# Performance work log

Measured on AMD Instinct MI355X. Metric: run time of the kernel, lower is better.

Reference implementation:

```python
import jax, jax.numpy as jnp
import numpy as np

DIM = 1024
HEADS = 16
HEAD_DIM = 64
INNER = HEADS * HEAD_DIM  # 1024
B, N = 4, 2048
EPS = 1e-5


def setup_inputs() -> dict:
    key = jax.random.key(0)
    ks = jax.random.split(key, 5)
    x = jax.random.normal(ks[0], (B, N, DIM), dtype=jnp.float32)
    w_qkv = jax.random.normal(ks[1], (DIM, 3 * INNER), dtype=jnp.float32) * (DIM ** -0.5)
    w_out = jax.random.normal(ks[2], (INNER, DIM), dtype=jnp.float32) * (INNER ** -0.5)
    b_out = jax.random.normal(ks[3], (DIM,), dtype=jnp.float32) * 0.01
    ln_gamma = jnp.ones((DIM,), dtype=jnp.float32)
    ln_beta = jnp.zeros((DIM,), dtype=jnp.float32)
    return {"x": x, "w_qkv": w_qkv, "w_out": w_out, "b_out": b_out,
            "ln_gamma": ln_gamma, "ln_beta": ln_beta}


def reference(x, w_qkv, w_out, b_out, ln_gamma, ln_beta):
    scale = HEAD_DIM ** -0.5
    qkv = x @ w_qkv  # [b, n, 3*inner]
    q, k, v = jnp.split(qkv, 3, axis=-1)
    q = q * scale
    # [b, n, h*d] -> [b, h, n, d]
    def to_heads(t):
        b, n, _ = t.shape
        return t.reshape(b, n, HEADS, HEAD_DIM).transpose(0, 2, 1, 3)
    q, k, v = to_heads(q), to_heads(k), to_heads(v)
    scores = jnp.einsum('bhid,bhjd->bhij', q, k)
    attn = jax.nn.softmax(scores, axis=-1)  # max-subtraction (detached) is internal
    out = jnp.einsum('bhij,bhjd->bhid', attn, v)
    out = out.transpose(0, 2, 1, 3).reshape(x.shape[0], x.shape[1], INNER)
    out = out @ w_out + b_out
    # LayerNorm over last dim
    mu = out.mean(axis=-1, keepdims=True)
    var = out.var(axis=-1, keepdims=True)
    out = (out - mu) * jax.lax.rsqrt(var + EPS)
    return out * ln_gamma + ln_beta
```

## Files before the change

### kernel.cpp

```cpp
#include <hip/hip_runtime.h>


typedef __bf16 bf16;
typedef __bf16 bf16x4 __attribute__((ext_vector_type(4)));
typedef __bf16 bf16x8 __attribute__((ext_vector_type(8)));
typedef float f32x4 __attribute__((ext_vector_type(4)));
typedef float f32x16 __attribute__((ext_vector_type(16)));
typedef unsigned int u32x2 __attribute__((ext_vector_type(2)));
typedef unsigned int u32x4 __attribute__((ext_vector_type(4)));

#define QSCALE_LOG2E 0.18033688011112042f

#define GLOAD_LDS16(gp, lp)                                                   \
  __builtin_amdgcn_global_load_lds(                                           \
      (const __attribute__((address_space(1))) unsigned int*)(const void*)(gp), \
      (__attribute__((address_space(3))) unsigned int*)(void*)(lp), 16, 0, 0)

__device__ __forceinline__ float fexp2(float x) {
#if __has_builtin(__builtin_amdgcn_exp2f)
  return __builtin_amdgcn_exp2f(x);
#else
  return __expf(x * 0.6931471805599453f);
#endif
}

__device__ __forceinline__ unsigned pack2t(float lo, float hi) {
  return __builtin_amdgcn_perm(__float_as_uint(hi), __float_as_uint(lo), 0x07060302u);
}

__global__ __launch_bounds__(256) void cvt_k(const float* __restrict__ in,
                                             bf16* __restrict__ out) {
  const size_t i = ((size_t)blockIdx.x * 256 + threadIdx.x) * 8;
  float4 a = *(const float4*)(in + i);
  float4 b = *(const float4*)(in + i + 4);
  bf16x8 o = {(bf16)a.x, (bf16)a.y, (bf16)a.z, (bf16)a.w,
              (bf16)b.x, (bf16)b.y, (bf16)b.z, (bf16)b.w};
  *(bf16x8*)(out + i) = o;
}

__global__ __launch_bounds__(256) void transpose_k(const float* __restrict__ in,
                                                   bf16* __restrict__ out,
                                                   int Kd, int Nd) {
  __shared__ bf16 t[32][36];
  const int n0 = blockIdx.x * 32, k0 = blockIdx.y * 32;
  const int r = threadIdx.x >> 3, c4 = (threadIdx.x & 7) * 4;
  float4 v = *(const float4*)(in + (size_t)(k0 + r) * Nd + n0 + c4);
  t[c4 + 0][r] = (bf16)v.x; t[c4 + 1][r] = (bf16)v.y;
  t[c4 + 2][r] = (bf16)v.z; t[c4 + 3][r] = (bf16)v.w;
  __syncthreads();
  bf16x4 o = *(const bf16x4*)&t[r][c4];
  *(bf16x4*)(out + (size_t)(n0 + r) * Kd + k0 + c4) = o;
}

template <bool QKV>
__global__ __launch_bounds__(256) void gemm2(const bf16* __restrict__ A,
                                             const bf16* __restrict__ Bt,
                                             bf16* __restrict__ C,
                                             bf16* __restrict__ Vt) {
  __shared__ bf16 As[128][64];
  __shared__ bf16 Bs[128][64];
  const int tid = threadIdx.x;
  const int l = tid & 63, w = tid >> 6;
  const int g = l >> 4, q = l & 15, q7 = q & 7;
  const int wm = w >> 1, wn = w & 1;
  const int m0 = blockIdx.x * 128, n0 = blockIdx.y * 128;
  const int lr = tid >> 3;
  const int sc = ((tid & 7) ^ (lr & 7)) * 8;

  f32x4 acc[4][4] = {};

  for (int k0 = 0; k0 < 1024; k0 += 64) {
    __syncthreads();
#pragma unroll
    for (int k = 0; k < 4; k++) {
      GLOAD_LDS16(A + (size_t)(m0 + lr + k * 32) * 1024 + k0 + sc,
                  &As[0][0] + tid * 8 + k * 2048);
      GLOAD_LDS16(Bt + (size_t)(n0 + lr + k * 32) * 1024 + k0 + sc,
                  &Bs[0][0] + tid * 8 + k * 2048);
    }
    __syncthreads();

#pragma unroll
    for (int ks = 0; ks < 2; ks++) {
      bf16x8 af[4], bfr[4];
#pragma unroll
      for (int mi = 0; mi < 4; mi++) {
        const int R = wm * 64 + mi * 16 + q;
        af[mi] = *(const bf16x8*)((const char*)&As[0][0] + R * 128 +
                                  (((ks * 4 + g) ^ q7) << 4));
      }
#pragma unroll
      for (int ni = 0; ni < 4; ni++) {
        const int R = wn * 64 + ni * 16 + q;
        bfr[ni] = *(const bf16x8*)((const char*)&Bs[0][0] + R * 128 +
                                   (((ks * 4 + g) ^ q7) << 4));
      }
#pragma unroll
      for (int mi = 0; mi < 4; mi++)
#pragma unroll
        for (int ni = 0; ni < 4; ni++)
          acc[mi][ni] = __builtin_amdgcn_mfma_f32_16x16x32_bf16(af[mi], bfr[ni],
                                                                acc[mi][ni], 0, 0, 0);
    }
  }

  if (QKV && n0 >= 2048) {
#pragma unroll
    for (int mi = 0; mi < 4; mi++)
#pragma unroll
      for (int ni = 0; ni < 4; ni++) {
        const int vcol = n0 - 2048 + wn * 64 + ni * 16 + q;
        const int h = vcol >> 6, d = vcol & 63;
        const int t0 = m0 + wm * 64 + mi * 16 + g * 4;
        const int b = t0 >> 11, n = t0 & 2047;
        bf16x4 o = {(bf16)acc[mi][ni][0], (bf16)acc[mi][ni][1],
                    (bf16)acc[mi][ni][2], (bf16)acc[mi][ni][3]};
        *(bf16x4*)(Vt + ((size_t)(b * 16 + h) * 64 + d) * 2048 + n) = o;
      }
  } else {
    const int ldc = QKV ? 2048 : 1024;
    const float s = (QKV && n0 < 1024) ? QSCALE_LOG2E : 1.0f;
#pragma unroll
    for (int mi = 0; mi < 4; mi++)
#pragma unroll
      for (int ni = 0; ni < 4; ni++) {
        const int col = n0 + wn * 64 + ni * 16 + q;
#pragma unroll
        for (int r = 0; r < 4; r++) {
          const int row = m0 + wm * 64 + mi * 16 + g * 4 + r;
          C[(size_t)row * ldc + col] = (bf16)(acc[mi][ni][r] * s);
        }
      }
  }
}

__global__ __launch_bounds__(256, 3) void attn_k(const bf16* __restrict__ qk,
                                                 const bf16* __restrict__ vt,
                                                 bf16* __restrict__ aout) {
  __shared__ bf16 Ks[3][64][64];
  __shared__ bf16 Vs[3][64][64];
  const int tid = threadIdx.x;
  const int l = tid & 63, w = tid >> 6;
  const int q = l & 31, hi = l >> 5, q7 = q & 7;

  const int flat = blockIdx.x;
  const int logical = (flat & 7) * 128 + (flat >> 3);
  const int qt = logical & 15, bh = logical >> 4;
  const int h = bh & 15, b = bh >> 4;
  const int qbase = qt * 128 + w * 32;

  const bf16* Kg = qk + (size_t)(b * 2048) * 2048 + 1024 + h * 64;
  const bf16* Vg = vt + ((size_t)(b * 16 + h) * 64) * 2048;

  bf16x8 qf[4];
  {
    const bf16* Qr = qk + (size_t)(b * 2048 + qbase + q) * 2048 + h * 64 + hi * 8;
#pragma unroll
    for (int i = 0; i < 4; i++) qf[i] = *(const bf16x8*)(Qr + i * 16);
  }

  const int r0 = tid >> 3, sp0 = ((tid & 7) ^ (r0 & 7)) * 8;
  const int ub = (tid >> 6) << 9;
#define STAGE_KV(buf, kt)                                                       \
  do {                                                                          \
    bf16* kd = &Ks[buf][0][0];                                                  \
    bf16* vd = &Vs[buf][0][0];                                                  \
    GLOAD_LDS16(Kg + (size_t)((kt) + r0) * 2048 + sp0, kd + ub);                \
    GLOAD_LDS16(Vg + (size_t)r0 * 2048 + (kt) + sp0, vd + ub);                  \
    GLOAD_LDS16(Kg + (size_t)((kt) + 32 + r0) * 2048 + sp0, kd + 2048 + ub);    \
    GLOAD_LDS16(Vg + (size_t)(32 + r0) * 2048 + (kt) + sp0, vd + 2048 + ub);    \
  } while (0)

#define QKT(buf, sA, sB)                                                        \
  do {                                                                          \
    const char* Kb_ = (const char*)&Ks[buf][0][0];                              \
    __builtin_amdgcn_s_setprio(1);                                              \
    {                                                                           \
      f32x16 a_ = {};                                                           \
      _Pragma("unroll")                                                         \
      for (int i = 0; i < 4; i++) {                                             \
        bf16x8 kf = *(const bf16x8*)(Kb_ + q * 128 + (((2 * i + hi) ^ q7) << 4));\
        a_ = __builtin_amdgcn_mfma_f32_32x32x16_bf16(kf, qf[i], a_, 0, 0, 0);   \
      }                                                                         \
      sA = a_;                                                                  \
    }                                                                           \
    {                                                                           \
      f32x16 a_ = {};                                                           \
      _Pragma("unroll")                                                         \
      for (int i = 0; i < 4; i++) {                                             \
        bf16x8 kf = *(const bf16x8*)(Kb_ + (32 + q) * 128 +                     \
                                     (((2 * i + hi) ^ q7) << 4));               \
        a_ = __builtin_amdgcn_mfma_f32_32x32x16_bf16(kf, qf[i], a_, 0, 0, 0);   \
      }                                                                         \
      sB = a_;                                                                  \
    }                                                                           \
    __builtin_amdgcn_s_setprio(0);                                              \
  } while (0)

  f32x16 oacc[2] = {};
  float lsA = 0.f, lsB = 0.f;

  STAGE_KV(0, 0);
  STAGE_KV(1, 64);
  asm volatile("s_waitcnt vmcnt(4)" ::: "memory");
  __builtin_amdgcn_sched_barrier(0);
  __builtin_amdgcn_s_barrier();

  f32x16 s0, s1;
  QKT(0, s0, s1);

  int cur = 0;
  for (int kt = 0; kt < 2048; kt += 64) {
    const int nbuf = (cur == 2) ? 0 : cur + 1;
    const int sbuf = (nbuf == 2) ? 0 : nbuf + 1;

    asm volatile("s_waitcnt vmcnt(0)" ::: "memory");
    __builtin_amdgcn_sched_barrier(0);
    __builtin_amdgcn_s_barrier();

    if (kt + 128 < 2048) STAGE_KV(sbuf, kt + 128);

    f32x16 n0v, n1v;
    QKT(nbuf, n0v, n1v);

#pragma unroll
    for (int r = 0; r < 16; r++) { s0[r] = fexp2(s0[r]); lsA += s0[r]; }
#pragma unroll
    for (int r = 0; r < 16; r++) { s1[r] = fexp2(s1[r]); lsB += s1[r]; }

    bf16x8 pfrag[4];
#pragma unroll
    for (int ks = 0; ks < 2; ks++) {
      const unsigned a0 = pack2t(s0[8 * ks + 0], s0[8 * ks + 1]);
      const unsigned a1 = pack2t(s0[8 * ks + 2], s0[8 * ks + 3]);
      const unsigned b0 = pack2t(s0[8 * ks + 4], s0[8 * ks + 5]);
      const unsigned b1 = pack2t(s0[8 * ks + 6], s0[8 * ks + 7]);
      u32x2 w0 = __builtin_amdgcn_permlane32_swap(a0, b0, false, false);
      u32x2 w1 = __builtin_amdgcn_permlane32_swap(a1, b1, false, false);
      u32x4 bw = {w0[0], w1[0], w0[1], w1[1]};
      pfrag[ks] = __builtin_bit_cast(bf16x8, bw);
    }
#pragma unroll
    for (int ks = 0; ks < 2; ks++) {
      const unsigned a0 = pack2t(s1[8 * ks + 0], s1[8 * ks + 1]);
      const unsigned a1 = pack2t(s1[8 * ks + 2], s1[8 * ks + 3]);
      const unsigned b0 = pack2t(s1[8 * ks + 4], s1[8 * ks + 5]);
      const unsigned b1 = pack2t(s1[8 * ks + 6], s1[8 * ks + 7]);
      u32x2 w0 = __builtin_amdgcn_permlane32_swap(a0, b0, false, false);
      u32x2 w1 = __builtin_amdgcn_permlane32_swap(a1, b1, false, false);
      u32x4 bw = {w0[0], w1[0], w0[1], w1[1]};
      pfrag[2 + ks] = __builtin_bit_cast(bf16x8, bw);
    }

    const char* Vb = (const char*)&Vs[cur][0][0];
    __builtin_amdgcn_s_setprio(1);
#pragma unroll
    for (int dblk = 0; dblk < 2; dblk++) {
      bf16x8 vfr[4];
#pragma unroll
      for (int t = 0; t < 4; t++)
        vfr[t] = *(const bf16x8*)(Vb + (dblk * 32 + q) * 128 + (((2 * t + hi) ^ q7) << 4));
#pragma unroll
      for (int t = 0; t < 4; t++)
        oacc[dblk] = __builtin_amdgcn_mfma_f32_32x32x16_bf16(vfr[t], pfrag[t],
                                                             oacc[dblk], 0, 0, 0);
    }
    __builtin_amdgcn_s_setprio(0);

    s0 = n0v; s1 = n1v;
    cur = nbuf;
  }

  float lsum = lsA + lsB;
  {
    u32x2 t2 = __builtin_amdgcn_permlane32_swap(__float_as_uint(lsum),
                                                __float_as_uint(lsum), false, false);
    lsum = __uint_as_float(t2[0]) + __uint_as_float(t2[1]);
  }
  const float inv = 1.f / lsum;
  bf16* orow = aout + (size_t)(b * 2048 + qbase + q) * 1024 + h * 64 + hi * 4;
#pragma unroll
  for (int dblk = 0; dblk < 2; dblk++)
#pragma unroll
    for (int rg = 0; rg < 4; rg++) {
      bf16x4 o = {(bf16)(oacc[dblk][4 * rg + 0] * inv), (bf16)(oacc[dblk][4 * rg + 1] * inv),
                  (bf16)(oacc[dblk][4 * rg + 2] * inv), (bf16)(oacc[dblk][4 * rg + 3] * inv)};
      *(bf16x4*)(orow + dblk * 32 + rg * 8) = o;
    }
#undef QKT
#undef STAGE_KV
}

__global__ __launch_bounds__(256) void ln_k(const bf16* __restrict__ proj,
                                            const float* __restrict__ bo,
                                            const float* __restrict__ gam,
                                            const float* __restrict__ bet,
                                            float* __restrict__ out) {
  const int tid = threadIdx.x;
  const int l = tid & 63, w = tid >> 6;
  const int row = blockIdx.x * 4 + w;
  const int c0 = l * 16;

  bf16x8 p0 = *(const bf16x8*)(proj + (size_t)row * 1024 + c0);
  bf16x8 p1 = *(const bf16x8*)(proj + (size_t)row * 1024 + c0 + 8);
  float v[16];
#pragma unroll
  for (int j = 0; j < 8; j++) { v[j] = (float)p0[j]; v[8 + j] = (float)p1[j]; }
#pragma unroll
  for (int j = 0; j < 4; j++) {
    float4 bv = *(const float4*)(bo + c0 + j * 4);
    v[4 * j + 0] += bv.x; v[4 * j + 1] += bv.y;
    v[4 * j + 2] += bv.z; v[4 * j + 3] += bv.w;
  }
  float s = 0.f, ss = 0.f;
#pragma unroll
  for (int j = 0; j < 16; j++) { s += v[j]; ss += v[j] * v[j]; }
#pragma unroll
  for (int off = 32; off > 0; off >>= 1) {
    s += __shfl_xor(s, off);
    ss += __shfl_xor(ss, off);
  }
  const float mean = s * (1.f / 1024.f);
  const float var = ss * (1.f / 1024.f) - mean * mean;
  const float rs = rsqrtf(var + 1e-5f);
#pragma unroll
  for (int j = 0; j < 4; j++) {
    float4 gv = *(const float4*)(gam + c0 + j * 4);
    float4 btv = *(const float4*)(bet + c0 + j * 4);
    float4 o;
    o.x = (v[4 * j + 0] - mean) * rs * gv.x + btv.x;
    o.y = (v[4 * j + 1] - mean) * rs * gv.y + btv.y;
    o.z = (v[4 * j + 2] - mean) * rs * gv.z + btv.z;
    o.w = (v[4 * j + 3] - mean) * rs * gv.w + btv.w;
    *(float4*)(out + (size_t)row * 1024 + c0 + j * 4) = o;
  }
}

extern "C" void kernel_launch(void* const* d_in, const int* in_sizes, int n_in,
                              void* d_out, int out_size, void* d_ws, size_t ws_size,
                              hipStream_t stream) {
  const float* x      = (const float*)d_in[0];
  const float* w_qkv  = (const float*)d_in[1];
  const float* w_out  = (const float*)d_in[2];
  const float* b_out  = (const float*)d_in[3];
  const float* gamma  = (const float*)d_in[4];
  const float* beta   = (const float*)d_in[5];
  float* out = (float*)d_out;

  char* ws = (char*)d_ws;
  bf16* xbf   = (bf16*)(ws);
  bf16* wqkvT = (bf16*)(ws + 16777216);
  bf16* woutT = (bf16*)(ws + 23068672);
  bf16* qkbuf = (bf16*)(ws + 25165824);
  bf16* vt    = (bf16*)(ws + 58720256);
  bf16* aout  = xbf;
  bf16* proj  = vt;

  dim3 blk(256);
  cvt_k<<<4096, blk, 0, stream>>>(x, xbf);
  transpose_k<<<dim3(96, 32), blk, 0, stream>>>(w_qkv, wqkvT, 1024, 3072);
  transpose_k<<<dim3(32, 32), blk, 0, stream>>>(w_out, woutT, 1024, 1024);
  gemm2<true><<<dim3(64, 24), blk, 0, stream>>>(xbf, wqkvT, qkbuf, vt);
  attn_k<<<1024, blk, 0, stream>>>(qkbuf, vt, aout);
  gemm2<false><<<dim3(64, 8), blk, 0, stream>>>(aout, woutT, proj, nullptr);
  ln_k<<<2048, blk, 0, stream>>>(proj, b_out, gamma, beta, out);
}
```

Before: 205.5 us.

## Triple-buffer GEMM K-tiles with async global-to-LDS prefetch

The GEMM main loop moves from a single 64-wide K tile with two barriers per iteration to a three-stage ring of 32-wide K tiles. Loads for the tile two steps ahead are issued before computing the current one, and progress is tracked with vmcnt waits and one barrier per step. The goal is to overlap global-to-LDS transfers with MFMA work instead of stalling on each load. In exchange it drops the XOR swizzle, which may add LDS bank conflicts on the 64-byte rows, and it halves the MFMAs per barrier.

```diff
diff --git a/kernel.cpp b/kernel.cpp
--- a/kernel.cpp
+++ b/kernel.cpp
@@ -57,51 +57,59 @@
                                              const bf16* __restrict__ Bt,
                                              bf16* __restrict__ C,
                                              bf16* __restrict__ Vt) {
-  __shared__ bf16 As[128][64];
-  __shared__ bf16 Bs[128][64];
+  __shared__ bf16 As[3][128][32];
+  __shared__ bf16 Bs[3][128][32];
   const int tid = threadIdx.x;
   const int l = tid & 63, w = tid >> 6;
-  const int g = l >> 4, q = l & 15, q7 = q & 7;
+  const int g = l >> 4, q = l & 15;
   const int wm = w >> 1, wn = w & 1;
   const int m0 = blockIdx.x * 128, n0 = blockIdx.y * 128;
-  const int lr = tid >> 3;
-  const int sc = ((tid & 7) ^ (lr & 7)) * 8;
+  const int lr = l >> 2, lc = (l & 3) * 8;
 
   f32x4 acc[4][4] = {};
 
-  for (int k0 = 0; k0 < 1024; k0 += 64) {
-    __syncthreads();
-#pragma unroll
-    for (int k = 0; k < 4; k++) {
-      GLOAD_LDS16(A + (size_t)(m0 + lr + k * 32) * 1024 + k0 + sc,
-                  &As[0][0] + tid * 8 + k * 2048);
-      GLOAD_LDS16(Bt + (size_t)(n0 + lr + k * 32) * 1024 + k0 + sc,
-                  &Bs[0][0] + tid * 8 + k * 2048);
-    }
-    __syncthreads();
-
-#pragma unroll
-    for (int ks = 0; ks < 2; ks++) {
-      bf16x8 af[4], bfr[4];
-#pragma unroll
-      for (int mi = 0; mi < 4; mi++) {
-        const int R = wm * 64 + mi * 16 + q;
-        af[mi] = *(const bf16x8*)((const char*)&As[0][0] + R * 128 +
-                                  (((ks * 4 + g) ^ q7) << 4));
-      }
-#pragma unroll
-      for (int ni = 0; ni < 4; ni++) {
-        const int R = wn * 64 + ni * 16 + q;
-        bfr[ni] = *(const bf16x8*)((const char*)&Bs[0][0] + R * 128 +
-                                   (((ks * 4 + g) ^ q7) << 4));
-      }
-#pragma unroll
-      for (int mi = 0; mi < 4; mi++)
-#pragma unroll
-        for (int ni = 0; ni < 4; ni++)
-          acc[mi][ni] = __builtin_amdgcn_mfma_f32_16x16x32_bf16(af[mi], bfr[ni],
-                                                                acc[mi][ni], 0, 0, 0);
-    }
+#define GSTAGE(buf, k0)                                                         \
+  do {                                                                          \
+    _Pragma("unroll")                                                           \
+    for (int i = 0; i < 2; i++) {                                               \
+      const int c = w + i * 4;                                                  \
+      GLOAD_LDS16(A + (size_t)(m0 + c * 16 + lr) * 1024 + (k0) + lc,            \
+                  &As[buf][c * 16][0]);                                         \
+      GLOAD_LDS16(Bt + (size_t)(n0 + c * 16 + lr) * 1024 + (k0) + lc,           \
+                  &Bs[buf][c * 16][0]);                                         \
+    }                                                                           \
+  } while (0)
+
+  GSTAGE(0, 0);
+  GSTAGE(1, 32);
+  int cur = 0, nxt2 = 2;
+
+  for (int k0 = 0; k0 < 1024; k0 += 32) {
+    if (k0 == 992) {
+      asm volatile("s_waitcnt vmcnt(0)" ::: "memory");
+    } else {
+      asm volatile("s_waitcnt vmcnt(4)" ::: "memory");
+    }
+    __builtin_amdgcn_sched_barrier(0);
+    __builtin_amdgcn_s_barrier();
+
+    if (k0 + 64 < 1024) GSTAGE(nxt2, k0 + 64);
+
+    bf16x8 af[4], bfr[4];
+#pragma unroll
+    for (int mi = 0; mi < 4; mi++)
+      af[mi] = *(const bf16x8*)&As[cur][wm * 64 + mi * 16 + q][g * 8];
+#pragma unroll
+    for (int ni = 0; ni < 4; ni++)
+      bfr[ni] = *(const bf16x8*)&Bs[cur][wn * 64 + ni * 16 + q][g * 8];
+#pragma unroll
+    for (int mi = 0; mi < 4; mi++)
+#pragma unroll
+      for (int ni = 0; ni < 4; ni++)
+        acc[mi][ni] = __builtin_amdgcn_mfma_f32_16x16x32_bf16(af[mi], bfr[ni], acc[mi][ni], 0, 0, 0);
+
+    cur = (cur == 2) ? 0 : cur + 1;
+    nxt2 = (nxt2 == 2) ? 0 : nxt2 + 1;
   }
 
   if (QKV && n0 >= 2048) {
@@ -132,6 +140,7 @@
         }
       }
   }
+#undef GSTAGE
 }
 
 __global__ __launch_bounds__(256, 3) void attn_k(const bf16* __restrict__ qk,
```

After: 208.1 us. About the same (+1.3%).
